# Performance work log

Hardware: AMD Instinct MI355X
Metric: run time of the kernel (lower is better)

Reference implementation:

```python
import jax, jax.numpy as jnp
import numpy as np

DN = ('NCHW', 'OIHW', 'NCHW')
K = 7          # window_size
PAD = K // 2   # 3
GC = 32
CIN = 1
COUT = 3
DIM = 128
RED = DIM // 4  # reduction=4 -> 32


def conv3x3(x, w, b):
    out = jax.lax.conv_general_dilated(x, w, (1, 1), [(1, 1), (1, 1)],
                                       dimension_numbers=DN)
    return out + b[None, :, None, None]


def lrelu(x):
    return jnp.where(x >= 0, x, 0.2 * x)


def setup_inputs() -> dict:
    key = jax.random.key(0)
    ks = jax.random.split(key, 18)
    def n(k, shape, s=0.05):
        return jax.random.normal(k, shape, dtype=jnp.float32) * s
    return {
        'x': jax.random.normal(ks[0], (8, CIN, 256, 256), dtype=jnp.float32),
        'c1_w': n(ks[1], (GC, CIN, 3, 3)),            'c1_b': n(ks[2], (GC,)),
        'c2_w': n(ks[3], (GC, CIN + GC, 3, 3)),       'c2_b': n(ks[4], (GC,)),
        'c3_w': n(ks[5], (GC, CIN + 2 * GC, 3, 3)),   'c3_b': n(ks[6], (GC,)),
        'c4_w': n(ks[7], (GC - 1, CIN + 3 * GC, 3, 3)), 'c4_b': n(ks[8], (GC - 1,)),
        # DynamicDWConv squeeze-excite weight generator
        'dw_w1': n(ks[9], (RED, DIM)),                # 1x1 conv, no bias
        'dw_bn_g': jnp.ones((RED,), jnp.float32),      # BN gamma (eval mode)
        'dw_bn_b': jnp.zeros((RED,), jnp.float32),     # BN beta
        'dw_w2': n(ks[10], (DIM * K * K, RED)),        'dw_b2': n(ks[11], (DIM * K * K,)),
        'dw_bias': n(ks[12], (DIM,)),                  # per-channel bias of depthwise conv
        'c5_w': n(ks[13], (COUT, DIM, 3, 3)),          'c5_b': n(ks[14], (COUT,)),
    }


def reference(x, c1_w, c1_b, c2_w, c2_b, c3_w, c3_b, c4_w, c4_b,
              dw_w1, dw_bn_g, dw_bn_b, dw_w2, dw_b2, dw_bias, c5_w, c5_b):
    # residual dense block
    x1 = lrelu(conv3x3(x, c1_w, c1_b))
    x2 = lrelu(conv3x3(jnp.concatenate((x, x1), 1), c2_w, c2_b))
    x3 = lrelu(conv3x3(jnp.concatenate((x, x1, x2), 1), c3_w, c3_b))
    x4 = lrelu(conv3x3(jnp.concatenate((x, x1, x2, x3), 1), c4_w, c4_b))
    feat = jnp.concatenate((x, x1, x2, x3, x4), 1)  # [b, 128, h, w]
    b = feat.shape[0]

    # DynamicDWConv: generate per-sample depthwise kernels via squeeze-excite
    pooled = feat.mean(axis=(2, 3))                            # [b, 128]
    h = jax.nn.relu(pooled @ dw_w1.T * dw_bn_g + dw_bn_b)      # BN(eval: mean=0,var=1)
    wgen = h @ dw_w2.T + dw_b2                                 # [b, 128*K*K]
    wdw = wgen.reshape(b, DIM, 1, K, K)                        # per-sample dw kernels

    def dw_one(xi, wi):  # xi: [128,h,w], wi: [128,1,K,K]
        return jax.lax.conv_general_dilated(
            xi[None], wi, (1, 1), [(PAD, PAD), (PAD, PAD)],
            dimension_numbers=DN, feature_group_count=DIM)[0]

    dw_out = jax.vmap(dw_one)(feat, wdw) + dw_bias[None, :, None, None]
    x45 = lrelu(dw_out)
    return conv3x3(x45, c5_w, c5_b)
```

## Files before the change

### kernel.cpp

```cpp
#include <hip/hip_runtime.h>
#include <hip/hip_bf16.h>


typedef _Float16 f16;
typedef _Float16 f16x2 __attribute__((ext_vector_type(2)));
typedef _Float16 f16x8 __attribute__((ext_vector_type(8)));
typedef float f32x16 __attribute__((ext_vector_type(16)));

#define IMG 256
#define HW 65536
#define CH 128

static __device__ __forceinline__ size_t fidx(int b, int h, int w) {
    return (((size_t)b * IMG + h) * IMG + w) * CH;
}

static __device__ __forceinline__ void lds_barrier() {
    asm volatile("s_waitcnt lgkmcnt(0)" ::: "memory");
    __builtin_amdgcn_s_barrier();
}

__global__ __launch_bounds__(256) void prep_wt_k(const float* __restrict__ src,
                                                 f16* __restrict__ dst,
                                                 int Cin, int COUT) {
    int idx = blockIdx.x * 256 + threadIdx.x;
    if (idx >= 9 * 32 * 128) return;
    int tap = idx >> 12;
    int oc  = (idx >> 7) & 31;
    int pc  = idx & 127;
    int ic  = (pc == 127) ? 0 : pc + 1;
    float v = 0.f;
    if (oc < COUT && ic < Cin) v = src[(oc * Cin + ic) * 9 + tap];
    dst[idx] = (f16)v;
}

__global__ __launch_bounds__(256) void conv1_k(const float* __restrict__ x,
                                               f16* __restrict__ feat,
                                               const float* __restrict__ w,
                                               const float* __restrict__ bias) {
    int wx = threadIdx.x, h = blockIdx.x & 255, b = blockIdx.x >> 8;
    const float* p = x + (size_t)b * HW + h * IMG;
    bool hm = h > 0, hp = h < 255, wm = wx > 0, wp = wx < 255;
    float v[9];
    v[0] = (hm && wm) ? p[wx - 1 - IMG] : 0.f;
    v[1] = hm ? p[wx - IMG] : 0.f;
    v[2] = (hm && wp) ? p[wx + 1 - IMG] : 0.f;
    v[3] = wm ? p[wx - 1] : 0.f;
    v[4] = p[wx];
    v[5] = wp ? p[wx + 1] : 0.f;
    v[6] = (hp && wm) ? p[wx - 1 + IMG] : 0.f;
    v[7] = hp ? p[wx + IMG] : 0.f;
    v[8] = (hp && wp) ? p[wx + 1 + IMG] : 0.f;

    float acc[32];
#pragma unroll
    for (int oc = 0; oc < 32; ++oc) {
        float s = bias[oc];
#pragma unroll
        for (int k = 0; k < 9; ++k) s = fmaf(v[k], w[oc * 9 + k], s);
        acc[oc] = (s >= 0.f) ? s : 0.2f * s;
    }
    f16* op = feat + fidx(b, h, wx);
#pragma unroll
    for (int oc = 0; oc < 32; oc += 2) {
        f16x2 pr = {(f16)acc[oc], (f16)acc[oc + 1]};
        *(f16x2*)(op + oc) = pr;
    }
    op[127] = (f16)v[4];
}

#define NSTT 10
#define STT (18 * 34 * 32)

__device__ __forceinline__ void stage_issue_t(const f16* __restrict__ src,
                                              int b, int r0, int w0, int c0,
                                              int tid, f16x8* v) {
#pragma unroll
    for (int it = 0; it < NSTT; ++it) {
        int u = tid + it * 256;
        int r = u / 136, rem = u - r * 136;
        int slot = rem >> 2, cg = rem & 3;
        int gh = r0 - 1 + r, gw = w0 - 1 + slot;
        bool ok = (u < 2448) && ((unsigned)gh < 256u) && ((unsigned)gw < 256u);
        int ch = gh < 0 ? 0 : (gh > 255 ? 255 : gh);
        int cw = gw < 0 ? 0 : (gw > 255 ? 255 : gw);
        f16x8 t = *(const f16x8*)(src + fidx(b, ch, cw) + c0 + cg * 8);
        f16x8 z = {};
        v[it] = ok ? t : z;
    }
}

__device__ __forceinline__ void stage_write_t(f16* __restrict__ St, int tid,
                                              const f16x8* v) {
#pragma unroll
    for (int it = 0; it < NSTT; ++it) {
        int u = tid + it * 256;
        if (u < 2448) {
            int r = u / 136, rem = u - r * 136;
            int slot = rem >> 2, cg = rem & 3;
            *(f16x8*)(St + ((r * 34 + slot) * 4 + (cg ^ ((slot >> 1) & 3))) * 8) = v[it];
        }
    }
}

__device__ __forceinline__ void compute_t(const f16* __restrict__ St,
                                          const f16* __restrict__ Wt, int c0,
                                          int wave, int l31, int g,
                                          f32x16* acc) {
#pragma unroll
    for (int kx = 0; kx < 3; ++kx) {
        f16x8 A0[3], A1[3];
#pragma unroll
        for (int ky = 0; ky < 3; ++ky) {
            const f16* wp = Wt + ((ky * 3 + kx) * 32 + l31) * 128 + c0 + g * 8;
            A0[ky] = *(const f16x8*)(wp);
            A1[ky] = *(const f16x8*)(wp + 16);
        }
        int slot = l31 + kx;
        int sw = (slot >> 1) & 3;
        int base = wave * 4;
        f16x8 B0[3], B1[3];
#pragma unroll
        for (int i = 0; i < 2; ++i) {
            int rb = ((base + i) * 34 + slot) * 4;
            B0[i] = *(const f16x8*)(St + (rb + ((0 + g) ^ sw)) * 8);
            B1[i] = *(const f16x8*)(St + (rb + ((2 + g) ^ sw)) * 8);
        }
#pragma unroll
        for (int r = 0; r < 4; ++r) {
            int rb = ((base + r + 2) * 34 + slot) * 4;
            B0[(r + 2) % 3] = *(const f16x8*)(St + (rb + ((0 + g) ^ sw)) * 8);
            B1[(r + 2) % 3] = *(const f16x8*)(St + (rb + ((2 + g) ^ sw)) * 8);
#pragma unroll
            for (int ky = 0; ky < 3; ++ky) {
                acc[r] = __builtin_amdgcn_mfma_f32_32x32x16_f16(A0[ky], B0[(r + ky) % 3], acc[r], 0, 0, 0);
                acc[r] = __builtin_amdgcn_mfma_f32_32x32x16_f16(A1[ky], B1[(r + ky) % 3], acc[r], 0, 0, 0);
            }
        }
    }
}

__global__ __launch_bounds__(256, 2) void convm_k(f16* __restrict__ feat,
                                                  const f16* __restrict__ Wt,
                                                  const float* __restrict__ bias,
                                                  int outbase, int cmask, int COUT) {
    __shared__ f16 St[2][STT];
    int tid = threadIdx.x;
    int wave = tid >> 6, lane = tid & 63;
    int l31 = lane & 31, g = lane >> 5;
    int bi = blockIdx.x;
    int b = bi & 7;
    int tile = bi >> 3;
    int pxt = tile & 7, rt = tile >> 3;
    int r0 = rt * 16;
    int w0 = pxt * 32;
    f32x16 acc[4] = {{}, {}, {}, {}};

    int cks[4], ncs = 0;
#pragma unroll
    for (int i = 0; i < 4; ++i)
        if ((cmask >> i) & 1) cks[ncs++] = i;

    {
        f16x8 v[NSTT];
        stage_issue_t(feat, b, r0, w0, cks[0] * 32, tid, v);
        stage_write_t(St[0], tid, v);
    }
    lds_barrier();

    for (int i = 0; i < ncs; ++i) {
        f16x8 vn[NSTT];
        if (i + 1 < ncs)
            stage_issue_t(feat, b, r0, w0, cks[i + 1] * 32, tid, vn);
        compute_t(St[i & 1], Wt, cks[i] * 32, wave, l31, g, acc);
        if (i + 1 < ncs)
            stage_write_t(St[(i + 1) & 1], tid, vn);
        lds_barrier();
    }

    int px = w0 + l31;
#pragma unroll
    for (int r = 0; r < 4; ++r) {
        f16* op = feat + fidx(b, r0 + wave * 4 + r, px) + outbase;
#pragma unroll
        for (int q = 0; q < 16; q += 2) {
            int oc0 = (q & 3) + 8 * (q >> 2) + 4 * g;
            float b0v = bias[oc0];
            float b1v = (oc0 + 1 < COUT) ? bias[oc0 + 1] : 0.f;
            float v0 = acc[r][q] + b0v;
            float v1 = acc[r][q + 1] + b1v;
            v0 = (v0 >= 0.f) ? v0 : 0.2f * v0;
            v1 = (v1 >= 0.f) ? v1 : 0.2f * v1;
            if (oc0 + 1 < COUT) {
                f16x2 pr = {(f16)v0, (f16)v1};
                *(f16x2*)(op + oc0) = pr;
            } else if (oc0 < COUT) {
                op[oc0] = (f16)v0;
            }
        }
    }
}

__global__ __launch_bounds__(256, 2) void convm_out_k(const f16* __restrict__ x45,
                                                      const f16* __restrict__ Wt,
                                                      const float* __restrict__ bias,
                                                      float* __restrict__ out,
                                                      int b0) {
    __shared__ f16 St[2][STT];
    int tid = threadIdx.x;
    int wave = tid >> 6, lane = tid & 63;
    int l31 = lane & 31, g = lane >> 5;
    int bi = blockIdx.x;
    int bl = bi & 3;
    int tile = bi >> 2;
    int pxt = tile & 7, rt = tile >> 3;
    int r0 = rt * 16;
    int w0 = pxt * 32;
    f32x16 acc[4] = {{}, {}, {}, {}};

    {
        f16x8 v[NSTT];
        stage_issue_t(x45, bl, r0, w0, 0, tid, v);
        stage_write_t(St[0], tid, v);
    }
    lds_barrier();

    for (int i = 0; i < 4; ++i) {
        f16x8 vn[NSTT];
        if (i + 1 < 4)
            stage_issue_t(x45, bl, r0, w0, (i + 1) * 32, tid, vn);
        compute_t(St[i & 1], Wt, i * 32, wave, l31, g, acc);
        if (i + 1 < 4)
            stage_write_t(St[(i + 1) & 1], tid, vn);
        lds_barrier();
    }

    if (g == 0) {
        int gb = b0 + bl;
        int px = w0 + l31;
#pragma unroll
        for (int r = 0; r < 4; ++r) {
#pragma unroll
            for (int oc = 0; oc < 3; ++oc) {
                float vv = acc[r][oc] + bias[oc];
                out[((size_t)(gb * 3 + oc)) * HW
                    + (size_t)(r0 + wave * 4 + r) * IMG + px] = vv;
            }
        }
    }
}

__global__ __launch_bounds__(256, 4) void dw_k(const f16* __restrict__ feat,
                                               const float* __restrict__ wgen,
                                               const float* __restrict__ dwb,
                                               f16* __restrict__ x45,
                                               int b0) {
    int tid = threadIdx.x;
    int lane = tid & 63;
    int wv = tid >> 6;
    int c = (wv & 1) * 64 + lane;
    int colh = wv >> 1;

    int bi = blockIdx.x;
    int ct = bi & 31;
    int t2 = bi >> 5;
    int vt = t2 & 7;
    int bl = t2 >> 3;
    int gb = b0 + bl;
    int x0 = ct * 8 + colh * 4;
    int y0 = vt * 32;

    int lc = (c == 127) ? 0 : c + 1;
    const float* wp = wgen + gb * 6272 + lc;
    f16x2 wp2[7][4];
#pragma unroll
    for (int k = 0; k < 7; ++k) {
#pragma unroll
        for (int p = 0; p < 3; ++p) {
            f16x2 t = {(f16)wp[(k * 7 + 2 * p) * 128],
                       (f16)wp[(k * 7 + 2 * p + 1) * 128]};
            wp2[k][p] = t;
        }
        f16x2 t3 = {(f16)wp[(k * 7 + 6) * 128], (f16)0.f};
        wp2[k][3] = t3;
    }
    float bias = dwb[lc];

    const f16* fb = feat + (size_t)gb * HW * CH + c;
    f16* xb = x45 + (size_t)bl * HW * CH + c;

    int xo[10];
    bool xm[10];
#pragma unroll
    for (int i = 0; i < 10; ++i) {
        int gx = x0 - 3 + i;
        xm[i] = (unsigned)gx < 256u;
        int cx = gx < 0 ? 0 : (gx > 255 ? 255 : gx);
        xo[i] = cx * CH;
    }

    float a[7][4] = {};

    for (int yi = 0; yi < 40; yi += 2) {
        int gy0 = y0 - 3 + yi, gy1 = gy0 + 1;
        bool ym0 = (unsigned)gy0 < 256u, ym1 = (unsigned)gy1 < 256u;
        int cy0 = gy0 < 0 ? 0 : (gy0 > 255 ? 255 : gy0);
        int cy1 = gy1 < 0 ? 0 : (gy1 > 255 ? 255 : gy1);
        const f16* r0 = fb + (size_t)cy0 * IMG * CH;
        const f16* r1 = fb + (size_t)cy1 * IMG * CH;

        f16 u0[10], u1[10];
#pragma unroll
        for (int i = 0; i < 10; ++i) u0[i] = r0[xo[i]];
#pragma unroll
        for (int i = 0; i < 10; ++i) u1[i] = r1[xo[i]];
#pragma unroll
        for (int i = 0; i < 10; ++i) {
            if (!(ym0 && xm[i])) u0[i] = (f16)0.f;
            if (!(ym1 && xm[i])) u1[i] = (f16)0.f;
        }

        {
            f16x2 pe[5], po[5];
#pragma unroll
            for (int p = 0; p < 5; ++p) { f16x2 t = {u0[2 * p], u0[2 * p + 1]}; pe[p] = t; }
#pragma unroll
            for (int p = 0; p < 4; ++p) { f16x2 t = {u0[2 * p + 1], u0[2 * p + 2]}; po[p] = t; }
            { f16x2 t = {u0[9], (f16)0.f}; po[4] = t; }
#pragma unroll
            for (int k = 0; k < 7; ++k) {
                const int wr = 6 - k;
#pragma unroll
                for (int p = 0; p < 4; ++p) {
                    a[k][0] = __builtin_amdgcn_fdot2(pe[p],     wp2[wr][p], a[k][0], false);
                    a[k][1] = __builtin_amdgcn_fdot2(po[p],     wp2[wr][p], a[k][1], false);
                    a[k][2] = __builtin_amdgcn_fdot2(pe[p + 1], wp2[wr][p], a[k][2], false);
                    a[k][3] = __builtin_amdgcn_fdot2(po[p + 1], wp2[wr][p], a[k][3], false);
                }
            }
            if (yi >= 6 && yi < 38) {
                int yo = y0 + yi - 6;
#pragma unroll
                for (int j = 0; j < 4; ++j) {
                    float s = a[0][j] + bias;
                    s = (s >= 0.f) ? s : 0.2f * s;
                    xb[((size_t)yo * IMG + x0 + j) * CH] = (f16)s;
                }
            }
#pragma unroll
            for (int k = 0; k < 6; ++k)
#pragma unroll
                for (int j = 0; j < 4; ++j) a[k][j] = a[k + 1][j];
#pragma unroll
            for (int j = 0; j < 4; ++j) a[6][j] = 0.f;
        }

        {
            f16x2 pe[5], po[5];
#pragma unroll
            for (int p = 0; p < 5; ++p) { f16x2 t = {u1[2 * p], u1[2 * p + 1]}; pe[p] = t; }
#pragma unroll
            for (int p = 0; p < 4; ++p) { f16x2 t = {u1[2 * p + 1], u1[2 * p + 2]}; po[p] = t; }
            { f16x2 t = {u1[9], (f16)0.f}; po[4] = t; }
#pragma unroll
            for (int k = 0; k < 7; ++k) {
                const int wr = 6 - k;
#pragma unroll
                for (int p = 0; p < 4; ++p) {
                    a[k][0] = __builtin_amdgcn_fdot2(pe[p],     wp2[wr][p], a[k][0], false);
                    a[k][1] = __builtin_amdgcn_fdot2(po[p],     wp2[wr][p], a[k][1], false);
                    a[k][2] = __builtin_amdgcn_fdot2(pe[p + 1], wp2[wr][p], a[k][2], false);
                    a[k][3] = __builtin_amdgcn_fdot2(po[p + 1], wp2[wr][p], a[k][3], false);
                }
            }
            int yib = yi + 1;
            if (yib >= 6 && yib < 38) {
                int yo = y0 + yib - 6;
#pragma unroll
                for (int j = 0; j < 4; ++j) {
                    float s = a[0][j] + bias;
                    s = (s >= 0.f) ? s : 0.2f * s;
                    xb[((size_t)yo * IMG + x0 + j) * CH] = (f16)s;
                }
            }
#pragma unroll
            for (int k = 0; k < 6; ++k)
#pragma unroll
                for (int j = 0; j < 4; ++j) a[k][j] = a[k + 1][j];
#pragma unroll
            for (int j = 0; j < 4; ++j) a[6][j] = 0.f;
        }
    }
}

__global__ __launch_bounds__(256) void pool_part_k(const f16* __restrict__ feat,
                                                   float* __restrict__ part) {
    __shared__ float red[4][128];
    int bi = blockIdx.x;
    int b = bi >> 5, pb = bi & 31;
    int t = threadIdx.x;
    int cp = t & 63, ps = t >> 6;
    int px0 = pb * 2048 + ps * 512;
    float s0 = 0.f, s1 = 0.f;
    const f16* base = feat + (size_t)b * HW * CH + (size_t)px0 * CH + cp * 2;
    for (int i = 0; i < 512; ++i) {
        f16x2 v = *(const f16x2*)(base + (size_t)i * CH);
        s0 += (float)v[0];
        s1 += (float)v[1];
    }
    red[ps][cp * 2] = s0;
    red[ps][cp * 2 + 1] = s1;
    __syncthreads();
    if (t < 128) {
        float s = red[0][t] + red[1][t] + red[2][t] + red[3][t];
        part[((size_t)b * 32 + pb) * 128 + t] = s;
    }
}

__global__ __launch_bounds__(256) void pool_fin_k(const float* __restrict__ part,
                                                  float* __restrict__ pooled) {
    int gid = blockIdx.x * 256 + threadIdx.x;
    if (gid >= 1024) return;
    int b = gid >> 7, pc = gid & 127;
    float s = 0.f;
    for (int pb = 0; pb < 32; ++pb) s += part[((size_t)b * 32 + pb) * 128 + pc];
    int lc = (pc == 127) ? 0 : pc + 1;
    pooled[b * 128 + lc] = s * (1.f / 65536.f);
}

__global__ __launch_bounds__(256) void mlp1_k(const float* __restrict__ pooled,
                                              const float* __restrict__ w1,
                                              const float* __restrict__ g,
                                              const float* __restrict__ bb,
                                              float* __restrict__ hbuf) {
    int t = threadIdx.x;
    int b = t >> 5, r = t & 31;
    float s = 0.f;
    for (int c = 0; c < 128; ++c) s += pooled[b * 128 + c] * w1[r * 128 + c];
    s = s * g[r] + bb[r];
    hbuf[t] = (s > 0.f) ? s : 0.f;
}

__global__ __launch_bounds__(256) void mlp2_k(const float* __restrict__ hbuf,
                                              const float* __restrict__ w2,
                                              const float* __restrict__ b2,
                                              float* __restrict__ wgen) {
    int idx = blockIdx.x * 256 + threadIdx.x;
    if (idx >= 8 * 6272) return;
    int b = idx / 6272, i = idx - b * 6272;
    float s = b2[i];
    for (int r = 0; r < 32; ++r) s += hbuf[b * 32 + r] * w2[i * 32 + r];
    int lc = i / 49, tp = i - lc * 49;
    wgen[b * 6272 + tp * 128 + lc] = s;
}

extern "C" void kernel_launch(void* const* d_in, const int* in_sizes, int n_in,
                              void* d_out, int out_size, void* d_ws, size_t ws_size,
                              hipStream_t stream) {
    (void)in_sizes; (void)n_in; (void)out_size; (void)ws_size;
    const float* x     = (const float*)d_in[0];
    const float* c1w   = (const float*)d_in[1];
    const float* c1b   = (const float*)d_in[2];
    const float* c2w   = (const float*)d_in[3];
    const float* c2b   = (const float*)d_in[4];
    const float* c3w   = (const float*)d_in[5];
    const float* c3b   = (const float*)d_in[6];
    const float* c4w   = (const float*)d_in[7];
    const float* c4b   = (const float*)d_in[8];
    const float* dw_w1 = (const float*)d_in[9];
    const float* bn_g  = (const float*)d_in[10];
    const float* bn_b  = (const float*)d_in[11];
    const float* dw_w2 = (const float*)d_in[12];
    const float* dw_b2 = (const float*)d_in[13];
    const float* dwb   = (const float*)d_in[14];
    const float* c5w   = (const float*)d_in[15];
    const float* c5b   = (const float*)d_in[16];
    float* out = (float*)d_out;

    f16* feat = (f16*)d_ws;
    f16* x45  = feat + (size_t)8 * HW * CH;
    f16* Wt   = x45 + (size_t)4 * HW * CH;
    f16* Wt2 = Wt, *Wt3 = Wt + 36864, *Wt4 = Wt + 73728, *Wt5 = Wt + 110592;
    float* part   = (float*)(Wt + 4 * 36864);
    float* pooled = part + 8 * 32 * 128;
    float* hbuf   = pooled + 1024;
    float* wgen   = hbuf + 256;

    prep_wt_k<<<144, 256, 0, stream>>>(c2w, Wt2, 33, 32);
    prep_wt_k<<<144, 256, 0, stream>>>(c3w, Wt3, 65, 32);
    prep_wt_k<<<144, 256, 0, stream>>>(c4w, Wt4, 97, 31);
    prep_wt_k<<<144, 256, 0, stream>>>(c5w, Wt5, 128, 3);

    conv1_k<<<2048, 256, 0, stream>>>(x, feat, c1w, c1b);
    convm_k<<<1024, 256, 0, stream>>>(feat, Wt2, c2b, 32, 0b1001, 32);
    convm_k<<<1024, 256, 0, stream>>>(feat, Wt3, c3b, 64, 0b1011, 32);
    convm_k<<<1024, 256, 0, stream>>>(feat, Wt4, c4b, 96, 0b1111, 31);

    pool_part_k<<<256, 256, 0, stream>>>(feat, part);
    pool_fin_k<<<4, 256, 0, stream>>>(part, pooled);
    mlp1_k<<<1, 256, 0, stream>>>(pooled, dw_w1, bn_g, bn_b, hbuf);
    mlp2_k<<<196, 256, 0, stream>>>(hbuf, dw_w2, dw_b2, wgen);

    for (int b0 = 0; b0 < 8; b0 += 4) {
        dw_k<<<1024, 256, 0, stream>>>(feat, wgen, dwb, x45, b0);
        convm_out_k<<<512, 256, 0, stream>>>(x45, Wt5, c5b, out, b0);
    }
}
```

Before: 463.9 us.

## Fuse dynamic depthwise conv with final 3x3 conv via LDS halo tile

```diff
diff --git a/kernel.cpp b/kernel.cpp
--- a/kernel.cpp
+++ b/kernel.cpp
@@ -201,76 +201,40 @@
     }
 }
 
-__global__ __launch_bounds__(256, 2) void convm_out_k(const f16* __restrict__ x45,
-                                                      const f16* __restrict__ Wt,
-                                                      const float* __restrict__ bias,
-                                                      float* __restrict__ out,
-                                                      int b0) {
-    __shared__ f16 St[2][STT];
+__global__ __launch_bounds__(256, 2) void dwc5f_k(const f16* __restrict__ feat,
+                                                  const float* __restrict__ wgen,
+                                                  const float* __restrict__ dwb,
+                                                  const float* __restrict__ c5w,
+                                                  const float* __restrict__ c5b,
+                                                  float* __restrict__ out,
+                                                  int b0) {
+    __shared__ __attribute__((aligned(16))) f16 Xt[4][180 * 32];
+    __shared__ __attribute__((aligned(16))) f16 W5i[4][864];
+
     int tid = threadIdx.x;
-    int wave = tid >> 6, lane = tid & 63;
-    int l31 = lane & 31, g = lane >> 5;
-    int bi = blockIdx.x;
-    int bl = bi & 3;
-    int tile = bi >> 2;
-    int pxt = tile & 7, rt = tile >> 3;
-    int r0 = rt * 16;
-    int w0 = pxt * 32;
-    f32x16 acc[4] = {{}, {}, {}, {}};
-
-    {
-        f16x8 v[NSTT];
-        stage_issue_t(x45, bl, r0, w0, 0, tid, v);
-        stage_write_t(St[0], tid, v);
-    }
-    lds_barrier();
-
-    for (int i = 0; i < 4; ++i) {
-        f16x8 vn[NSTT];
-        if (i + 1 < 4)
-            stage_issue_t(x45, bl, r0, w0, (i + 1) * 32, tid, vn);
-        compute_t(St[i & 1], Wt, i * 32, wave, l31, g, acc);
-        if (i + 1 < 4)
-            stage_write_t(St[(i + 1) & 1], tid, vn);
-        lds_barrier();
-    }
-
-    if (g == 0) {
-        int gb = b0 + bl;
-        int px = w0 + l31;
-#pragma unroll
-        for (int r = 0; r < 4; ++r) {
-#pragma unroll
-            for (int oc = 0; oc < 3; ++oc) {
-                float vv = acc[r][oc] + bias[oc];
-                out[((size_t)(gb * 3 + oc)) * HW
-                    + (size_t)(r0 + wave * 4 + r) * IMG + px] = vv;
-            }
-        }
-    }
-}
-
-__global__ __launch_bounds__(256, 4) void dw_k(const f16* __restrict__ feat,
-                                               const float* __restrict__ wgen,
-                                               const float* __restrict__ dwb,
-                                               f16* __restrict__ x45,
-                                               int b0) {
-    int tid = threadIdx.x;
-    int lane = tid & 63;
-    int wv = tid >> 6;
-    int c = (wv & 1) * 64 + lane;
-    int colh = wv >> 1;
-
     int bi = blockIdx.x;
     int ct = bi & 31;
     int t2 = bi >> 5;
-    int vt = t2 & 7;
-    int bl = t2 >> 3;
+    int rt = t2 & 15;
+    int bl = t2 >> 4;
     int gb = b0 + bl;
-    int x0 = ct * 8 + colh * 4;
-    int y0 = vt * 32;
-
+    int x0 = ct * 8, y0 = rt * 16;
+
+    for (int i = tid; i < 3456; i += 256) {
+        int ck = i / 864, r2 = i - ck * 864;
+        int oc = r2 / 288, r3 = r2 - oc * 288;
+        int tp = r3 >> 5, cc = r3 & 31;
+        int pc = ck * 32 + cc;
+        int lc = (pc == 127) ? 0 : pc + 1;
+        W5i[ck][oc * 288 + tp * 32 + cc] = (f16)c5w[(oc * 128 + lc) * 9 + tp];
+    }
+
+    int lane = tid & 63, wv = tid >> 6;
+    int c = (wv & 1) * 64 + lane;
+    int colh = wv >> 1;
+    int cl = c & 31, ckc = c >> 5;
     int lc = (c == 127) ? 0 : c + 1;
+
     const float* wp = wgen + gb * 6272 + lc;
     f16x2 wp2[7][4];
 #pragma unroll
@@ -287,46 +251,47 @@
     float bias = dwb[lc];
 
     const f16* fb = feat + (size_t)gb * HW * CH + c;
-    f16* xb = x45 + (size_t)bl * HW * CH + c;
-
-    int xo[10];
-    bool xm[10];
-#pragma unroll
-    for (int i = 0; i < 10; ++i) {
-        int gx = x0 - 3 + i;
+    int co0 = x0 - 1 + colh * 5;
+
+    int xo[11];
+    bool xm[11];
+#pragma unroll
+    for (int i = 0; i < 11; ++i) {
+        int gx = co0 - 3 + i;
         xm[i] = (unsigned)gx < 256u;
         int cx = gx < 0 ? 0 : (gx > 255 ? 255 : gx);
         xo[i] = cx * CH;
     }
 
-    float a[7][4] = {};
-
-    for (int yi = 0; yi < 40; yi += 2) {
-        int gy0 = y0 - 3 + yi, gy1 = gy0 + 1;
+    float a[7][5] = {};
+
+    for (int yi = 0; yi < 24; yi += 2) {
+        int gy0 = y0 - 4 + yi, gy1 = gy0 + 1;
         bool ym0 = (unsigned)gy0 < 256u, ym1 = (unsigned)gy1 < 256u;
         int cy0 = gy0 < 0 ? 0 : (gy0 > 255 ? 255 : gy0);
         int cy1 = gy1 < 0 ? 0 : (gy1 > 255 ? 255 : gy1);
-        const f16* r0 = fb + (size_t)cy0 * IMG * CH;
-        const f16* r1 = fb + (size_t)cy1 * IMG * CH;
-
-        f16 u0[10], u1[10];
-#pragma unroll
-        for (int i = 0; i < 10; ++i) u0[i] = r0[xo[i]];
-#pragma unroll
-        for (int i = 0; i < 10; ++i) u1[i] = r1[xo[i]];
-#pragma unroll
-        for (int i = 0; i < 10; ++i) {
+        const f16* r0p = fb + (size_t)cy0 * IMG * CH;
+        const f16* r1p = fb + (size_t)cy1 * IMG * CH;
+
+        f16 u0[12], u1[12];
+#pragma unroll
+        for (int i = 0; i < 11; ++i) u0[i] = r0p[xo[i]];
+#pragma unroll
+        for (int i = 0; i < 11; ++i) u1[i] = r1p[xo[i]];
+#pragma unroll
+        for (int i = 0; i < 11; ++i) {
             if (!(ym0 && xm[i])) u0[i] = (f16)0.f;
             if (!(ym1 && xm[i])) u1[i] = (f16)0.f;
         }
+        u0[11] = (f16)0.f;
+        u1[11] = (f16)0.f;
 
         {
-            f16x2 pe[5], po[5];
-#pragma unroll
-            for (int p = 0; p < 5; ++p) { f16x2 t = {u0[2 * p], u0[2 * p + 1]}; pe[p] = t; }
-#pragma unroll
-            for (int p = 0; p < 4; ++p) { f16x2 t = {u0[2 * p + 1], u0[2 * p + 2]}; po[p] = t; }
-            { f16x2 t = {u0[9], (f16)0.f}; po[4] = t; }
+            f16x2 pe[6], po[5];
+#pragma unroll
+            for (int p = 0; p < 6; ++p) { f16x2 t = {u0[2 * p], u0[2 * p + 1]}; pe[p] = t; }
+#pragma unroll
+            for (int p = 0; p < 5; ++p) { f16x2 t = {u0[2 * p + 1], u0[2 * p + 2]}; po[p] = t; }
 #pragma unroll
             for (int k = 0; k < 7; ++k) {
                 const int wr = 6 - k;
@@ -336,32 +301,37 @@
                     a[k][1] = __builtin_amdgcn_fdot2(po[p],     wp2[wr][p], a[k][1], false);
                     a[k][2] = __builtin_amdgcn_fdot2(pe[p + 1], wp2[wr][p], a[k][2], false);
                     a[k][3] = __builtin_amdgcn_fdot2(po[p + 1], wp2[wr][p], a[k][3], false);
+                    a[k][4] = __builtin_amdgcn_fdot2(pe[p + 2], wp2[wr][p], a[k][4], false);
                 }
             }
-            if (yi >= 6 && yi < 38) {
-                int yo = y0 + yi - 6;
-#pragma unroll
-                for (int j = 0; j < 4; ++j) {
+            if (yi >= 6) {
+                int yl = yi - 6;
+                int gy = y0 - 1 + yl;
+                bool yok = (unsigned)gy < 256u;
+#pragma unroll
+                for (int j = 0; j < 5; ++j) {
                     float s = a[0][j] + bias;
                     s = (s >= 0.f) ? s : 0.2f * s;
-                    xb[((size_t)yo * IMG + x0 + j) * CH] = (f16)s;
+                    int gx = co0 + j;
+                    if (!yok || (unsigned)gx >= 256u) s = 0.f;
+                    int pxl = yl * 10 + colh * 5 + j;
+                    Xt[ckc][(pxl * 4 + ((cl >> 3) ^ (pxl & 3))) * 8 + (cl & 7)] = (f16)s;
                 }
             }
 #pragma unroll
             for (int k = 0; k < 6; ++k)
 #pragma unroll
-                for (int j = 0; j < 4; ++j) a[k][j] = a[k + 1][j];
-#pragma unroll
-            for (int j = 0; j < 4; ++j) a[6][j] = 0.f;
+                for (int j = 0; j < 5; ++j) a[k][j] = a[k + 1][j];
+#pragma unroll
+            for (int j = 0; j < 5; ++j) a[6][j] = 0.f;
         }
 
         {
-            f16x2 pe[5], po[5];
-#pragma unroll
-            for (int p = 0; p < 5; ++p) { f16x2 t = {u1[2 * p], u1[2 * p + 1]}; pe[p] = t; }
-#pragma unroll
-            for (int p = 0; p < 4; ++p) { f16x2 t = {u1[2 * p + 1], u1[2 * p + 2]}; po[p] = t; }
-            { f16x2 t = {u1[9], (f16)0.f}; po[4] = t; }
+            f16x2 pe[6], po[5];
+#pragma unroll
+            for (int p = 0; p < 6; ++p) { f16x2 t = {u1[2 * p], u1[2 * p + 1]}; pe[p] = t; }
+#pragma unroll
+            for (int p = 0; p < 5; ++p) { f16x2 t = {u1[2 * p + 1], u1[2 * p + 2]}; po[p] = t; }
 #pragma unroll
             for (int k = 0; k < 7; ++k) {
                 const int wr = 6 - k;
@@ -371,25 +341,66 @@
                     a[k][1] = __builtin_amdgcn_fdot2(po[p],     wp2[wr][p], a[k][1], false);
                     a[k][2] = __builtin_amdgcn_fdot2(pe[p + 1], wp2[wr][p], a[k][2], false);
                     a[k][3] = __builtin_amdgcn_fdot2(po[p + 1], wp2[wr][p], a[k][3], false);
+                    a[k][4] = __builtin_amdgcn_fdot2(pe[p + 2], wp2[wr][p], a[k][4], false);
                 }
             }
             int yib = yi + 1;
-            if (yib >= 6 && yib < 38) {
-                int yo = y0 + yib - 6;
-#pragma unroll
-                for (int j = 0; j < 4; ++j) {
+            if (yib >= 6) {
+                int yl = yib - 6;
+                int gy = y0 - 1 + yl;
+                bool yok = (unsigned)gy < 256u;
+#pragma unroll
+                for (int j = 0; j < 5; ++j) {
                     float s = a[0][j] + bias;
                     s = (s >= 0.f) ? s : 0.2f * s;
-                    xb[((size_t)yo * IMG + x0 + j) * CH] = (f16)s;
+                    int gx = co0 + j;
+                    if (!yok || (unsigned)gx >= 256u) s = 0.f;
+                    int pxl = yl * 10 + colh * 5 + j;
+                    Xt[ckc][(pxl * 4 + ((cl >> 3) ^ (pxl & 3))) * 8 + (cl & 7)] = (f16)s;
                 }
             }
 #pragma unroll
             for (int k = 0; k < 6; ++k)
 #pragma unroll
-                for (int j = 0; j < 4; ++j) a[k][j] = a[k + 1][j];
-#pragma unroll
-            for (int j = 0; j < 4; ++j) a[6][j] = 0.f;
-        }
+                for (int j = 0; j < 5; ++j) a[k][j] = a[k + 1][j];
+#pragma unroll
+            for (int j = 0; j < 5; ++j) a[6][j] = 0.f;
+        }
+    }
+
+    __syncthreads();
+
+    if (tid < 128) {
+        int r = tid >> 3, col = tid & 7;
+        float acc[3] = {0.f, 0.f, 0.f};
+#pragma unroll
+        for (int ck = 0; ck < 4; ++ck) {
+#pragma unroll
+            for (int tap = 0; tap < 9; ++tap) {
+                int ky = tap / 3, kx = tap - ky * 3;
+                int pxl = (r + ky) * 10 + (col + kx);
+                int sw = pxl & 3;
+#pragma unroll
+                for (int g2 = 0; g2 < 4; ++g2) {
+                    f16x8 xv = *(const f16x8*)(&Xt[ck][(pxl * 4 + (g2 ^ sw)) * 8]);
+#pragma unroll
+                    for (int oc = 0; oc < 3; ++oc) {
+                        const f16* wv5 = &W5i[ck][oc * 288 + tap * 32 + g2 * 8];
+                        f16x8 wv = *(const f16x8*)(wv5);
+#pragma unroll
+                        for (int p2 = 0; p2 < 4; ++p2) {
+                            f16x2 xp = {xv[2 * p2], xv[2 * p2 + 1]};
+                            f16x2 wpp = {wv[2 * p2], wv[2 * p2 + 1]};
+                            acc[oc] = __builtin_amdgcn_fdot2(xp, wpp, acc[oc], false);
+                        }
+                    }
+                }
+            }
+        }
+        size_t ob = ((size_t)gb * 3) * HW + (size_t)(y0 + r) * IMG + (x0 + col);
+        out[ob]          = acc[0] + c5b[0];
+        out[ob + HW]     = acc[1] + c5b[1];
+        out[ob + 2 * HW] = acc[2] + c5b[2];
     }
 }
 
@@ -478,10 +489,9 @@
     float* out = (float*)d_out;
 
     f16* feat = (f16*)d_ws;
-    f16* x45  = feat + (size_t)8 * HW * CH;
-    f16* Wt   = x45 + (size_t)4 * HW * CH;
-    f16* Wt2 = Wt, *Wt3 = Wt + 36864, *Wt4 = Wt + 73728, *Wt5 = Wt + 110592;
-    float* part   = (float*)(Wt + 4 * 36864);
+    f16* Wt   = feat + (size_t)8 * HW * CH;
+    f16* Wt2 = Wt, *Wt3 = Wt + 36864, *Wt4 = Wt + 73728;
+    float* part   = (float*)(Wt + 3 * 36864);
     float* pooled = part + 8 * 32 * 128;
     float* hbuf   = pooled + 1024;
     float* wgen   = hbuf + 256;
@@ -489,7 +499,6 @@
     prep_wt_k<<<144, 256, 0, stream>>>(c2w, Wt2, 33, 32);
     prep_wt_k<<<144, 256, 0, stream>>>(c3w, Wt3, 65, 32);
     prep_wt_k<<<144, 256, 0, stream>>>(c4w, Wt4, 97, 31);
-    prep_wt_k<<<144, 256, 0, stream>>>(c5w, Wt5, 128, 3);
 
     conv1_k<<<2048, 256, 0, stream>>>(x, feat, c1w, c1b);
     convm_k<<<1024, 256, 0, stream>>>(feat, Wt2, c2b, 32, 0b1001, 32);
@@ -501,8 +510,6 @@
     mlp1_k<<<1, 256, 0, stream>>>(pooled, dw_w1, bn_g, bn_b, hbuf);
     mlp2_k<<<196, 256, 0, stream>>>(hbuf, dw_w2, dw_b2, wgen);
 
-    for (int b0 = 0; b0 < 8; b0 += 4) {
-        dw_k<<<1024, 256, 0, stream>>>(feat, wgen, dwb, x45, b0);
-        convm_out_k<<<512, 256, 0, stream>>>(x45, Wt5, c5b, out, b0);
-    }
-}
+    for (int b0 = 0; b0 < 8; b0 += 4)
+        dwc5f_k<<<2048, 256, 0, stream>>>(feat, wgen, dwb, c5w, c5b, out, b0);
+}
```

Result: slower. 509.8 us (+9.9%).
